# Kernel tuning notes

Hardware: AMD Instinct MI355X
Metric: run time of the kernel (lower is better)

The kernel has to match this reference:

```python
import jax, jax.numpy as jnp
import numpy as np

OUTLINER_RATIO = 0.01
RANK = 16
SVD_NITER = 2  # matches torch.svd_lowrank default


def _randomized_svd(A, rank, key, niter=SVD_NITER):
    # torch.svd_lowrank-style randomized range finder + small SVD.
    n, d = A.shape
    Omega = jax.random.normal(key, (d, rank), dtype=A.dtype)
    Q, _ = jnp.linalg.qr(A @ Omega)               # [n, rank]
    for _ in range(niter):
        Q, _ = jnp.linalg.qr(A.T @ Q)             # [d, rank]
        Q, _ = jnp.linalg.qr(A @ Q)               # [n, rank]
    B = Q.T @ A                                   # [rank, d]
    Ub, S, Vh = jnp.linalg.svd(B, full_matrices=False)
    U = Q @ Ub                                    # [n, rank]
    return U, S, Vh


def get_statistics(x, outliner_ratio):
    # threshold such that ~outliner_ratio fraction of |x| exceeds it
    return jnp.quantile(jnp.abs(x), 1.0 - outliner_ratio)


def compress(x, outliner, rank, key):
    # split outliers (kept exactly) from sub-outlier part (low-rank compressed)
    x_outlier = jnp.where(jnp.abs(x) > outliner, x, jnp.zeros((), x.dtype))
    x_sub = (x - x_outlier).reshape(-1, x.shape[-1])   # [N, D]
    U, S, Vh = _randomized_svd(x_sub, rank, key)
    R = Vh.T                                           # [D, rank]
    Rinv = Vh                                          # orthonormal -> pinv = transpose
    L = x_sub @ R                                      # [N, rank]
    return x_outlier, L, R, Rinv


def reference(x, iteration):
    result = jax.nn.silu(x)
    # iteration < 10 branch: compute fresh outlier statistics
    outliner = get_statistics(x, OUTLINER_RATIO)
    # iteration % 50 == 0 -> execute_svd = True (iteration = 0 here)
    key = jax.random.key(42)
    x_outlier_compressed, L, R, Rinv = compress(x, outliner, RANK, key)
    return result, outliner, R, Rinv


def setup_inputs() -> dict:
    key = jax.random.key(0)
    x = jax.random.normal(key, (4, 2048, 4096), dtype=jnp.float32)
    return {"x": x, "iteration": 0}
```

## Files before the change

kernel.cpp:

```cpp
#include <hip/hip_runtime.h>
#include <math.h>


#define N_TOTAL 33554432
#define DDIM    4096
#define NROWS   8192
#define NCHUNK  32
#define RTARGET 33218888u

__device__ __forceinline__ double frcp(double x){
  double r = (double)(1.0f/(float)x);
  r = r*(2.0 - x*r);
  r = r*(2.0 - x*r);
  return r;
}
__device__ __forceinline__ double frsqrt(double x){
  double r = (double)rsqrtf((float)x);
  double hx = 0.5*x;
  r = r*(1.5 - hx*r*r);
  r = r*(1.5 - hx*r*r);
  return r;
}
__device__ __forceinline__ double fsqrt(double x){
  return (x == 0.0) ? 0.0 : x*frsqrt(x);
}

__device__ __forceinline__ double dsign(double a, double b){ return (b >= 0.0) ? fabs(a) : -fabs(a); }

__device__ __forceinline__ void f_slartg(double f, double g, double& c, double& s, double& r){
  if (g == 0.0){ c=1.0; s=0.0; r=f; }
  else if (f == 0.0){ c=0.0; s=dsign(1.0,g); r=fabs(g); }
  else {
    double d2 = f*f+g*g;
    double inv = frsqrt(d2);
    c = fabs(f)*inv;
    r = dsign(d2*inv, f);
    s = g*inv*dsign(1.0,f);
  }
}

__device__ void f_slas2(double f, double g, double h, double& ssmin, double& ssmax){
  double fa=fabs(f), ga=fabs(g), ha=fabs(h);
  double fhmn=fmin(fa,ha), fhmx=fmax(fa,ha);
  if (fhmn == 0.0){
    ssmin=0.0;
    if (fhmx==0.0) ssmax=ga;
    else { double mx=fmax(fhmx,ga), mn=fmin(fhmx,ga); double q=mn*frcp(mx); ssmax = mx*fsqrt(1.0+q*q); }
  } else {
    if (ga < fhmx){
      double rinv = frcp(fhmx);
      double as_=1.0+fhmn*rinv, at=(fhmx-fhmn)*rinv, au=ga*rinv; au=au*au;
      double c=2.0*frcp(fsqrt(as_*as_+au)+fsqrt(at*at+au));
      ssmin=fhmn*c; ssmax=fhmx*frcp(c);
    } else {
      double au=fhmx*frcp(ga);
      if (au==0.0){ ssmin=(fhmn*fhmx)*frcp(ga); ssmax=ga; }
      else {
        double rinv = frcp(fhmx);
        double as_=1.0+fhmn*rinv, at=(fhmx-fhmn)*rinv;
        double c=frcp(fsqrt(1.0+(as_*au)*(as_*au))+fsqrt(1.0+(at*au)*(at*au)));
        ssmin=(fhmn*c)*au; ssmin=ssmin+ssmin; ssmax=ga*frcp(c+c);
      }
    }
  }
}

__device__ void f_slasv2(double f, double g, double h,
                         double& ssmin, double& ssmax, double& snr, double& csr, double& snl, double& csl){
  const double EPSd = 5.9604645e-8;
  double ft=f, fa=fabs(f), ht=h, ha=fabs(h);
  int pmax=1;
  bool swap_=(ha>fa);
  if (swap_){ pmax=3; double t=ft; ft=ht; ht=t; t=fa; fa=ha; ha=t; }
  double gt=g, ga=fabs(g);
  double clt=0, crt=0, slt=0, srt=0;
  if (ga == 0.0){ ssmin=ha; ssmax=fa; clt=1; crt=1; slt=0; srt=0; }
  else {
    bool gasmal=true;
    if (ga > fa){
      pmax=2;
      if ((fa*frcp(ga)) < EPSd){
        gasmal=false;
        ssmax=ga;
        ssmin = (ha>1.0) ? (fa*frcp(ga*frcp(ha))) : ((fa*frcp(ga))*ha);
        clt=1; slt=ht*frcp(gt); srt=1; crt=ft*frcp(gt);
      }
    }
    if (gasmal){
      double d_=fa-ha;
      double fainv = frcp(fa);
      double l_=(d_==fa)?1.0:(d_*fainv);
      double m_=gt*frcp(ft);
      double t_=2.0-l_;
      double mm=m_*m_, tt=t_*t_;
      double s_=fsqrt(tt+mm);
      double r_=(l_==0.0)?fabs(m_):fsqrt(l_*l_+mm);
      double a_=0.5*(s_+r_);
      double ainv = frcp(a_);
      ssmin=ha*ainv;
      ssmax=fa*a_;
      if (mm==0.0){
        t_=(l_==0.0)?(dsign(2.0,ft)*dsign(1.0,gt)):(gt*frcp(dsign(d_,ft))+m_*frcp(t_));
      } else {
        t_=(m_*frcp(s_+t_)+m_*frcp(r_+l_))*(1.0+a_);
      }
      l_=fsqrt(t_*t_+4.0);
      double linv = frcp(l_);
      crt=2.0*linv;
      srt=t_*linv;
      clt=(crt+srt*m_)*ainv;
      slt=(ht*frcp(ft))*srt*ainv;
    }
  }
  if (swap_){ csl=srt; snl=crt; csr=slt; snr=clt; }
  else { csl=clt; snl=slt; csr=crt; snr=srt; }
  double tsign=0.0;
  if (pmax==1) tsign = dsign(1.0,csr)*dsign(1.0,csl)*dsign(1.0,f);
  if (pmax==2) tsign = dsign(1.0,snr)*dsign(1.0,csl)*dsign(1.0,g);
  if (pmax==3) tsign = dsign(1.0,snr)*dsign(1.0,snl)*dsign(1.0,h);
  ssmax = dsign(ssmax, tsign);
  ssmin = dsign(ssmin, tsign*dsign(1.0,f)*dsign(1.0,h));
}

__global__ __launch_bounds__(256) void k_hist1(const float4* __restrict__ x4, unsigned* __restrict__ h1){
  __shared__ unsigned lh[4096];
  for (int i=threadIdx.x; i<4096; i+=256) lh[i]=0u;
  __syncthreads();
  int tid = blockIdx.x*blockDim.x + threadIdx.x;
  int stride = gridDim.x*blockDim.x;
  for (int i = tid; i < N_TOTAL/4; i += stride){
    float4 v = x4[i];
    atomicAdd(&lh[(__float_as_uint(v.x)&0x7FFFFFFFu)>>19], 1u);
    atomicAdd(&lh[(__float_as_uint(v.y)&0x7FFFFFFFu)>>19], 1u);
    atomicAdd(&lh[(__float_as_uint(v.z)&0x7FFFFFFFu)>>19], 1u);
    atomicAdd(&lh[(__float_as_uint(v.w)&0x7FFFFFFFu)>>19], 1u);
  }
  __syncthreads();
  for (int i=threadIdx.x; i<4096; i+=256){ unsigned c=lh[i]; if (c) atomicAdd(&h1[i], c); }
}

__global__ __launch_bounds__(1024) void k_select1(const unsigned* __restrict__ h1, unsigned* __restrict__ sel){
  __shared__ unsigned ssum[1024];
  int t = threadIdx.x;
  unsigned psum = 0;
  for (int k=0;k<4;++k) psum += h1[t*4+k];
  ssum[t]=psum; __syncthreads();
  for (int off=1; off<1024; off<<=1){
    unsigned v = (t>=off)? ssum[t-off]:0u;
    __syncthreads();
    ssum[t] += v;
    __syncthreads();
  }
  unsigned incl = ssum[t], excl = incl - psum;
  if (excl <= RTARGET && RTARGET < incl){
    unsigned run = excl;
    for (int k=0;k<4;++k){
      unsigned c = h1[t*4+k];
      if (run + c > RTARGET){ sel[1]=(unsigned)(t*4+k); sel[2]=RTARGET-run; break; }
      run += c;
    }
  }
}

__global__ void k_hist2(const float4* __restrict__ x4, unsigned* __restrict__ h2, const unsigned* __restrict__ sel){
  unsigned hstar = sel[1];
  int tid = blockIdx.x*blockDim.x + threadIdx.x;
  int stride = gridDim.x*blockDim.x;
  for (int i = tid; i < N_TOTAL/4; i += stride){
    float4 v = x4[i];
    unsigned b;
    b = __float_as_uint(v.x) & 0x7FFFFFFFu; if ((b>>19)==hstar) atomicAdd(&h2[b&0x7FFFFu],1u);
    b = __float_as_uint(v.y) & 0x7FFFFFFFu; if ((b>>19)==hstar) atomicAdd(&h2[b&0x7FFFFu],1u);
    b = __float_as_uint(v.z) & 0x7FFFFFFFu; if ((b>>19)==hstar) atomicAdd(&h2[b&0x7FFFFu],1u);
    b = __float_as_uint(v.w) & 0x7FFFFFFFu; if ((b>>19)==hstar) atomicAdd(&h2[b&0x7FFFFu],1u);
  }
}

__global__ __launch_bounds__(128) void k_grpsum(const uint4* __restrict__ h2v, unsigned* __restrict__ gs){
  __shared__ unsigned red[128];
  int g = blockIdx.x, t = threadIdx.x;
  uint4 v = h2v[(size_t)g*128 + t];
  red[t] = v.x+v.y+v.z+v.w;
  __syncthreads();
  for (int off=64; off; off>>=1){ if (t<off) red[t] += red[t+off]; __syncthreads(); }
  if (t==0) gs[g] = red[0];
}

__global__ __launch_bounds__(1024) void k_select2b(const unsigned* __restrict__ gs, const unsigned* __restrict__ h2,
                                                   unsigned* __restrict__ sel, float* __restrict__ outScalar){
  __shared__ unsigned ssum[1024];
  __shared__ unsigned sg[2];
  int t = threadIdx.x;
  unsigned target = sel[2], hstar = sel[1];
  unsigned psum = gs[t];
  ssum[t]=psum; __syncthreads();
  for (int off=1; off<1024; off<<=1){
    unsigned v = (t>=off)? ssum[t-off]:0u;
    __syncthreads();
    ssum[t] += v;
    __syncthreads();
  }
  unsigned incl = ssum[t], excl = incl - psum;
  if (excl <= target && target < incl){ sg[0]=(unsigned)t; sg[1]=excl; }
  __syncthreads();
  unsigned g = sg[0], gexcl = sg[1];
  unsigned cnt = (t<512) ? h2[(size_t)g*512 + t] : 0u;
  __syncthreads();
  ssum[t]=cnt; __syncthreads();
  for (int off=1; off<1024; off<<=1){
    unsigned v = (t>=off)? ssum[t-off]:0u;
    __syncthreads();
    ssum[t] += v;
    __syncthreads();
  }
  unsigned incl2 = ssum[t], excl2 = incl2 - cnt;
  unsigned rem = target - gexcl;
  if (t < 512 && excl2 <= rem && rem < incl2){
    unsigned tb = (hstar<<19) | (g*512 + (unsigned)t);
    float tv = __uint_as_float(tb);
    ((float*)sel)[0] = tv;
    *outScalar = tv;
  }
}

__device__ __forceinline__ unsigned rotl32(unsigned x, int r){ return (x<<r)|(x>>(32-r)); }

__device__ __forceinline__ float bits_to_normal(unsigned g){
  float u01 = __uint_as_float((g>>9) | 0x3F800000u) - 1.0f;
  float u = __fadd_rn(__fmul_rn(u01, 2.0f), -0.99999994f);
  u = fmaxf(-0.99999994f, u);
  float xx = __fmul_rn(u,u);
  float w = -log1pf(-xx);
  float p;
  if (w < 5.0f){
    w = __fadd_rn(w, -2.5f);
    p = 2.81022636e-08f;
    p = __fadd_rn(3.43273939e-07f, __fmul_rn(p,w));
    p = __fadd_rn(-3.5233877e-06f, __fmul_rn(p,w));
    p = __fadd_rn(-4.39150654e-06f, __fmul_rn(p,w));
    p = __fadd_rn(0.00021858087f, __fmul_rn(p,w));
    p = __fadd_rn(-0.00125372503f, __fmul_rn(p,w));
    p = __fadd_rn(-0.00417768164f, __fmul_rn(p,w));
    p = __fadd_rn(0.246640727f, __fmul_rn(p,w));
    p = __fadd_rn(1.50140941f, __fmul_rn(p,w));
  } else {
    w = __fadd_rn(sqrtf(w), -3.0f);
    p = -0.000200214257f;
    p = __fadd_rn(0.000100950558f, __fmul_rn(p,w));
    p = __fadd_rn(0.00134934322f, __fmul_rn(p,w));
    p = __fadd_rn(-0.00367342844f, __fmul_rn(p,w));
    p = __fadd_rn(0.00573950773f, __fmul_rn(p,w));
    p = __fadd_rn(-0.0076224613f, __fmul_rn(p,w));
    p = __fadd_rn(0.00943887047f, __fmul_rn(p,w));
    p = __fadd_rn(1.00167406f, __fmul_rn(p,w));
    p = __fadd_rn(2.83297682f, __fmul_rn(p,w));
  }
  return __fmul_rn(__uint_as_float(0x3FB504F3u), __fmul_rn(p,u));
}

#define TF_ROUND(r) { x0 += x1; x1 = rotl32(x1,(r)); x1 ^= x0; }

__global__ void k_omega(float* __restrict__ om){
  unsigned p = blockIdx.x*blockDim.x + threadIdx.x;
  unsigned x0 = p, x1 = 32768u + p;
  const unsigned ks0 = 0u, ks1 = 42u, ks2 = 0x1BD11BDAu ^ 0u ^ 42u;
  x0 += ks0; x1 += ks1;
  TF_ROUND(13) TF_ROUND(15) TF_ROUND(26) TF_ROUND(6)   x0+=ks1; x1+=ks2+1u;
  TF_ROUND(17) TF_ROUND(29) TF_ROUND(16) TF_ROUND(24)  x0+=ks2; x1+=ks0+2u;
  TF_ROUND(13) TF_ROUND(15) TF_ROUND(26) TF_ROUND(6)   x0+=ks0; x1+=ks1+3u;
  TF_ROUND(17) TF_ROUND(29) TF_ROUND(16) TF_ROUND(24)  x0+=ks1; x1+=ks2+4u;
  TF_ROUND(13) TF_ROUND(15) TF_ROUND(26) TF_ROUND(6)   x0+=ks2; x1+=ks0+5u;
  om[p]         = bits_to_normal(x0);
  om[p+32768u]  = bits_to_normal(x1);
}

__global__ __launch_bounds__(256) void k_gemmA(const float* __restrict__ x, const float* __restrict__ W,
                                               float* __restrict__ Y, const float* __restrict__ sel){
  __shared__ double xs[16][128];
  __shared__ double ws[128][16];
  const float t = sel[0];
  const int tid = threadIdx.x;
  const int c = tid & 15, rl = tid >> 4;
  const int row0 = blockIdx.x*16;
  const int c8 = c*8;
  const int wk = (tid*8) >> 4, wc = (tid*8) & 15;
  double acc = 0.0;
  for (int kt = 0; kt < DDIM; kt += 128){
    const float4* p = (const float4*)(x + (size_t)(row0+rl)*DDIM + kt + c8);
    float4 a = p[0], b = p[1];
    xs[rl][c8+0] = (fabsf(a.x) > t) ? 0.0 : (double)a.x;
    xs[rl][c8+1] = (fabsf(a.y) > t) ? 0.0 : (double)a.y;
    xs[rl][c8+2] = (fabsf(a.z) > t) ? 0.0 : (double)a.z;
    xs[rl][c8+3] = (fabsf(a.w) > t) ? 0.0 : (double)a.w;
    xs[rl][c8+4] = (fabsf(b.x) > t) ? 0.0 : (double)b.x;
    xs[rl][c8+5] = (fabsf(b.y) > t) ? 0.0 : (double)b.y;
    xs[rl][c8+6] = (fabsf(b.z) > t) ? 0.0 : (double)b.z;
    xs[rl][c8+7] = (fabsf(b.w) > t) ? 0.0 : (double)b.w;
    const float4* q = (const float4*)(W + (size_t)kt*16 + tid*8);
    float4 wa = q[0], wb = q[1];
    ws[wk][wc+0]=(double)wa.x; ws[wk][wc+1]=(double)wa.y; ws[wk][wc+2]=(double)wa.z; ws[wk][wc+3]=(double)wa.w;
    ws[wk][wc+4]=(double)wb.x; ws[wk][wc+5]=(double)wb.y; ws[wk][wc+6]=(double)wb.z; ws[wk][wc+7]=(double)wb.w;
    __syncthreads();
    #pragma unroll 8
    for (int k=0;k<128;++k) acc += xs[rl][k]*ws[k][c];
    __syncthreads();
  }
  Y[(size_t)(row0+rl)*16 + c] = (float)acc;
}

__global__ __launch_bounds__(256) void k_gemmAT(const float* __restrict__ x, const float* __restrict__ Q,
                                                double* __restrict__ part, const float* __restrict__ sel){
  __shared__ double qs[128][16];
  const float t = sel[0];
  const int tid = threadIdx.x;
  const int d = blockIdx.x*256 + tid;
  const int chunk = blockIdx.y;
  const int i0 = chunk*(NROWS/NCHUNK);
  double acc[16];
  #pragma unroll
  for (int c=0;c<16;++c) acc[c]=0.0;
  for (int it=0; it<NROWS/NCHUNK; it+=128){
    {
      const float4* src = (const float4*)(Q + (size_t)(i0+it)*16) + tid*2;
      float4 a = src[0], b = src[1];
      double* dst = &qs[0][0] + tid*8;
      dst[0]=(double)a.x; dst[1]=(double)a.y; dst[2]=(double)a.z; dst[3]=(double)a.w;
      dst[4]=(double)b.x; dst[5]=(double)b.y; dst[6]=(double)b.z; dst[7]=(double)b.w;
    }
    __syncthreads();
    for (int ii=0; ii<128; ++ii){
      float xv = x[(size_t)(i0+it+ii)*DDIM + d];
      xv = (fabsf(xv) > t) ? 0.0f : xv;
      double xd = (double)xv;
      #pragma unroll
      for (int c=0;c<16;++c) acc[c] += xd*qs[ii][c];
    }
    __syncthreads();
  }
  double* pp = part + ((size_t)chunk*DDIM + d)*16;
  #pragma unroll
  for (int c=0;c<16;++c) pp[c]=acc[c];
}

__global__ void k_reduceT(const double* __restrict__ part, float* __restrict__ outM, int asB, int nchunks){
  int idx = blockIdx.x*blockDim.x + threadIdx.x;
  if (idx >= DDIM*16) return;
  double s = 0.0;
  for (int c=0;c<nchunks;++c) s += part[(size_t)c*DDIM*16 + idx];
  int d = idx >> 4, r = idx & 15;
  if (asB) outM[(size_t)r*DDIM + d] = (float)s;
  else     outM[idx] = (float)s;
}

__global__ __launch_bounds__(256) void k_gramM(const float* __restrict__ M, int rowsPerChunk,
                                               double* __restrict__ part){
  __shared__ float lds[16][17];
  int t = threadIdx.x; int i = t>>4, j = t&15;
  int r0 = blockIdx.x*rowsPerChunk;
  double acc = 0.0;
  for (int rt=0; rt<rowsPerChunk; rt+=16){
    lds[t>>4][t&15] = M[(size_t)(r0+rt+(t>>4))*16 + (t&15)];
    __syncthreads();
    #pragma unroll
    for (int dd=0; dd<16; ++dd) acc += (double)lds[dd][i]*(double)lds[dd][j];
    __syncthreads();
  }
  part[(size_t)blockIdx.x*256 + t] = acc;
}

__global__ __launch_bounds__(256) void k_gramB(const float* __restrict__ B, double* __restrict__ part){
  __shared__ float lds[16][17];
  int t = threadIdx.x; int i = t>>4, j = t&15;
  int d0 = blockIdx.x*256;
  double acc = 0.0;
  for (int dt=0; dt<256; dt+=16){
    lds[t>>4][t&15] = B[(size_t)(t>>4)*DDIM + d0+dt+(t&15)];
    __syncthreads();
    #pragma unroll
    for (int dd=0; dd<16; ++dd) acc += (double)lds[i][dd]*(double)lds[j][dd];
    __syncthreads();
  }
  part[(size_t)blockIdx.x*256 + t] = acc;
}

__global__ __launch_bounds__(256) void k_redchol(const double* __restrict__ part, int nchunks,
                                                 double* __restrict__ Lout, double* __restrict__ Uinv){
  __shared__ double Gs[16][17];
  __shared__ double Vs[16][17];
  int t = threadIdx.x;
  {
    double s = 0.0;
    for (int c=0;c<nchunks;++c) s += part[(size_t)c*256 + t];
    Gs[t>>4][t&15] = s;
  }
  __syncthreads();
  int l = t;
  for (int k=0;k<16;++k){
    if (l==k) Gs[k][k] = fsqrt(Gs[k][k]);
    __syncthreads();
    if (l>k && l<16) Gs[k][l] = Gs[k][l]*frcp(Gs[k][k]);
    __syncthreads();
    if (l>k && l<16){
      double g = Gs[k][l];
      for (int i=k+1;i<=l;++i) Gs[i][l] -= Gs[k][i]*g;
    }
    __syncthreads();
  }
  if (l<16){
    for (int i=0;i<16;++i) Vs[i][l] = 0.0;
    Vs[l][l] = frcp(Gs[l][l]);
    for (int i=l-1;i>=0;--i){
      double s = 0.0;
      for (int k=i+1;k<=l;++k) s += Gs[i][k]*Vs[k][l];
      Vs[i][l] = -s*frcp(Gs[i][i]);
    }
  }
  __syncthreads();
  if (l<16){
    for (int c=0;c<16;++c){
      Lout[l*16+c] = (c<=l) ? Gs[c][l] : 0.0;
      Uinv[l*16+c] = (l<=c) ? Vs[l][c] : 0.0;
    }
  }
}

__global__ __launch_bounds__(256) void k_applyRinv(float* __restrict__ M, const double* __restrict__ Uinv){
  __shared__ double su[256];
  int t = threadIdx.x;
  su[t] = Uinv[t];
  int r = blockIdx.x*16 + (t>>4);
  int j = t & 15;
  const float4* rp = (const float4*)(M + (size_t)r*16);
  float4 v0=rp[0], v1=rp[1], v2=rp[2], v3=rp[3];
  float rowv[16] = {v0.x,v0.y,v0.z,v0.w, v1.x,v1.y,v1.z,v1.w,
                    v2.x,v2.y,v2.z,v2.w, v3.x,v3.y,v3.z,v3.w};
  __syncthreads();
  double acc = 0.0;
  #pragma unroll
  for (int k=0;k<16;++k) acc += (double)rowv[k]*su[k*16+j];
  M[(size_t)r*16 + j] = (float)acc;
}

__global__ __launch_bounds__(64) void k_smallsvd(const double* __restrict__ Lg, double* __restrict__ Wout){
  __shared__ double Lm[16][16];
  __shared__ double VT[16][16];
  __shared__ double A1[16][16];
  __shared__ double dd[16], ee[16], tp[16];
  int l = threadIdx.x;
  for (int idx=l; idx<256; idx+=64){ int r=idx>>4, c=idx&15; Lm[r][c] = (c<=r)? Lg[r*16+c] : 0.0; }
  __syncthreads();
  for (int i=0;i<16;++i){
    double xn2=0.0;
    for (int r=i+1;r<16;++r){ double v=Lm[r][i]; xn2 += v*v; }
    double alpha = Lm[i][i];
    double beta, tauq_, scl;
    if (xn2==0.0){ tauq_=0.0; beta=alpha; scl=0.0; }
    else { beta = -dsign(fsqrt(alpha*alpha+xn2), alpha); tauq_=(beta-alpha)*frcp(beta); scl=frcp(alpha-beta); }
    __syncthreads();
    if (l>i && l<16) Lm[l][i] *= scl;
    __syncthreads();
    dd[i]=beta;
    if (tauq_ != 0.0 && l>i && l<16){
      int j=l;
      double w = Lm[i][j];
      for (int r=i+1;r<16;++r) w += Lm[r][i]*Lm[r][j];
      w *= tauq_;
      Lm[i][j] -= w;
      for (int r=i+1;r<16;++r) Lm[r][j] -= w*Lm[r][i];
    }
    __syncthreads();
    if (i<15){
      double xn2b=0.0;
      for (int c=i+2;c<16;++c){ double v=Lm[i][c]; xn2b+=v*v; }
      double alpha2=Lm[i][i+1];
      double beta2, taup_, scl2;
      if (xn2b==0.0){ taup_=0.0; beta2=alpha2; scl2=0.0; }
      else { beta2=-dsign(fsqrt(alpha2*alpha2+xn2b),alpha2); taup_=(beta2-alpha2)*frcp(beta2); scl2=frcp(alpha2-beta2); }
      __syncthreads();
      if (l>=i+2 && l<16) Lm[i][l] *= scl2;
      __syncthreads();
      ee[i]=beta2; tp[i]=taup_;
      if (taup_!=0.0 && l>i && l<16){
        int r=l;
        double w=Lm[r][i+1];
        for (int c=i+2;c<16;++c) w += Lm[i][c]*Lm[r][c];
        w *= taup_;
        Lm[r][i+1] -= w;
        for (int c=i+2;c<16;++c) Lm[r][c] -= w*Lm[i][c];
      }
      __syncthreads();
    } else { tp[i]=0.0; __syncthreads(); }
  }
  for (int idx=l; idx<256; idx+=64){ int r=idx>>4,c=idx&15; VT[r][c]=(r==c)?1.0:0.0; }
  __syncthreads();
  const double EPSs = 5.9604645e-8;
  const double UNFL = 1.17549435e-38;
  double tol = 10.0*EPSs;
  double sminoa, mu;
  sminoa = mu = fabs(dd[0]);
  if (sminoa != 0.0){
    for (int k=1;k<16;++k){ mu = fabs(dd[k])*(mu*frcp(mu+fabs(ee[k-1]))); sminoa=fmin(sminoa,mu); if (sminoa==0.0) break; }
  }
  sminoa = sminoa/4.0;
  double thresh = fmax(tol*sminoa, 6.0*16.0*16.0*UNFL);
  int m=16, oldll=-1, oldm=-1, idir=0;
  double sminl=0.0;
  int guard=0;
  #define Dv(k) dd[(k)-1]
  #define Ev(k) ee[(k)-1]
  while (m > 1 && guard < 3000){
    ++guard;
    int ll=0; bool split=false;
    double smax_=fabs(Dv(m)), smin_=smax_;
    for (int lll=1; lll<=m-1; ++lll){
      ll = m-lll;
      double abss=fabs(Dv(ll)), abse=fabs(Ev(ll));
      if (abse <= thresh){ split=true; break; }
      smin_=fmin(smin_,abss); smax_=fmax(smax_,fmax(abss,abse));
    }
    if (!split) ll=0;
    else {
      Ev(ll)=0.0;
      if (ll == m-1){ m = m-1; continue; }
    }
    ll = ll+1;
    if (ll == m-1){
      double sigmn,sigmx,sinr,cosr,sinl_,cosl;
      f_slasv2(Dv(m-1), Ev(m-1), Dv(m), sigmn, sigmx, sinr, cosr, sinl_, cosl);
      Dv(m-1)=sigmx; Ev(m-1)=0.0; Dv(m)=sigmn;
      if (l<16){
        double t0 = cosr*VT[m-2][l] + sinr*VT[m-1][l];
        VT[m-1][l] = cosr*VT[m-1][l] - sinr*VT[m-2][l];
        VT[m-2][l] = t0;
      }
      __syncthreads();
      m -= 2; continue;
    }
    if (ll > oldm || m < oldll) idir = (fabs(Dv(ll)) >= fabs(Dv(m))) ? 1 : 2;
    bool cont=false;
    if (idir==1){
      if (fabs(Ev(m-1)) <= tol*fabs(Dv(m))){ Ev(m-1)=0.0; continue; }
      mu = fabs(Dv(ll)); sminl=mu;
      for (int lll=ll; lll<=m-1; ++lll){
        if (fabs(Ev(lll)) <= tol*mu){ Ev(lll)=0.0; cont=true; break; }
        mu = fabs(Dv(lll+1))*(mu*frcp(mu+fabs(Ev(lll)))); sminl=fmin(sminl,mu);
      }
    } else {
      if (fabs(Ev(ll)) <= tol*fabs(Dv(ll))){ Ev(ll)=0.0; continue; }
      mu = fabs(Dv(m)); sminl=mu;
      for (int lll=m-1; lll>=ll; --lll){
        if (fabs(Ev(lll)) <= tol*mu){ Ev(lll)=0.0; cont=true; break; }
        mu = fabs(Dv(lll))*(mu*frcp(mu+fabs(Ev(lll)))); sminl=fmin(sminl,mu);
      }
    }
    if (cont) continue;
    oldll=ll; oldm=m;
    double shift=0.0, rdum;
    if (!( 16.0*tol*(sminl*frcp(smax_)) <= fmax(EPSs, 0.01*tol) )){
      double sll;
      if (idir==1){ sll=fabs(Dv(ll)); f_slas2(Dv(m-1), Ev(m-1), Dv(m), shift, rdum); }
      else        { sll=fabs(Dv(m));  f_slas2(Dv(ll), Ev(ll), Dv(ll+1), shift, rdum); }
      if (sll>0.0){ double q=shift*frcp(sll); if (q*q < EPSs) shift=0.0; }
    }
    if (shift == 0.0){
      if (idir==1){
        double cs=1.0, oldcs=1.0, oldsn=0.0, r_;
        for (int i1=ll;i1<=m-1;++i1){
          double cn, snn;
          double a0 = Dv(i1)*cs;
          f_slartg(a0, Ev(i1), cn, snn, r_);
          if (i1>ll) Ev(i1-1) = oldsn*r_;
          double ocn, osn, dnew;
          f_slartg(oldcs*r_, Dv(i1+1)*snn, ocn, osn, dnew);
          Dv(i1)=dnew;
          cs=cn; oldcs=ocn; oldsn=osn;
          if (l<16){
            double t0 = cs*VT[i1-1][l] + snn*VT[i1][l];
            VT[i1][l] = cs*VT[i1][l] - snn*VT[i1-1][l];
            VT[i1-1][l] = t0;
          }
        }
        double h=Dv(m)*cs;
        Dv(m)=h*oldcs; Ev(m-1)=h*oldsn;
        if (fabs(Ev(m-1))<=thresh) Ev(m-1)=0.0;
      } else {
        double cs=1.0, oldcs=1.0, oldsn=0.0, r_;
        for (int i1=m;i1>=ll+1;--i1){
          double cn,snn;
          double a0 = Dv(i1)*cs;
          f_slartg(a0, Ev(i1-1), cn, snn, r_);
          if (i1<m) Ev(i1)=oldsn*r_;
          double ocn,osn,dnew;
          f_slartg(oldcs*r_, Dv(i1-1)*snn, ocn, osn, dnew);
          Dv(i1)=dnew;
          cs=cn; oldcs=ocn; oldsn=osn;
          if (l<16){
            double c_=oldcs, s_=-oldsn;
            double t0 = c_*VT[i1-2][l] + s_*VT[i1-1][l];
            VT[i1-1][l] = c_*VT[i1-1][l] - s_*VT[i1-2][l];
            VT[i1-2][l] = t0;
          }
        }
        double h=Dv(ll)*cs;
        Dv(ll)=h*oldcs; Ev(ll)=h*oldsn;
        if (fabs(Ev(ll))<=thresh) Ev(ll)=0.0;
      }
    } else {
      if (idir==1){
        double f=(fabs(Dv(ll))-shift)*(dsign(1.0,Dv(ll))+shift*frcp(Dv(ll)));
        double g=Ev(ll);
        for (int i1=ll;i1<=m-1;++i1){
          double cosr,sinr,cosl,sinl_,r_;
          f_slartg(f,g,cosr,sinr,r_);
          if (i1>ll) Ev(i1-1)=r_;
          f = cosr*Dv(i1)+sinr*Ev(i1);
          Ev(i1) = cosr*Ev(i1)-sinr*Dv(i1);
          g = sinr*Dv(i1+1);
          Dv(i1+1) = cosr*Dv(i1+1);
          f_slartg(f,g,cosl,sinl_,r_);
          Dv(i1)=r_;
          f = cosl*Ev(i1)+sinl_*Dv(i1+1);
          Dv(i1+1) = cosl*Dv(i1+1)-sinl_*Ev(i1);
          if (i1 < m-1){ g = sinl_*Ev(i1+1); Ev(i1+1)=cosl*Ev(i1+1); }
          if (l<16){
            double t0 = cosr*VT[i1-1][l] + sinr*VT[i1][l];
            VT[i1][l] = cosr*VT[i1][l] - sinr*VT[i1-1][l];
            VT[i1-1][l] = t0;
          }
        }
        Ev(m-1)=f;
        if (fabs(Ev(m-1))<=thresh) Ev(m-1)=0.0;
      } else {
        double f=(fabs(Dv(m))-shift)*(dsign(1.0,Dv(m))+shift*frcp(Dv(m)));
        double g=Ev(m-1);
        for (int i1=m;i1>=ll+1;--i1){
          double cosr,sinr,cosl,sinl_,r_;
          f_slartg(f,g,cosr,sinr,r_);
          if (i1<m) Ev(i1)=r_;
          f = cosr*Dv(i1)+sinr*Ev(i1-1);
          Ev(i1-1)=cosr*Ev(i1-1)-sinr*Dv(i1);
          g = sinr*Dv(i1-1);
          Dv(i1-1)=cosr*Dv(i1-1);
          f_slartg(f,g,cosl,sinl_,r_);
          Dv(i1)=r_;
          f = cosl*Ev(i1-1)+sinl_*Dv(i1-1);
          Dv(i1-1)=cosl*Dv(i1-1)-sinl_*Ev(i1-1);
          if (i1 > ll+1){ g=sinl_*Ev(i1-2); Ev(i1-2)=cosl*Ev(i1-2); }
          if (l<16){
            double c_=cosr, s_=-sinr;
            double t0 = c_*VT[i1-2][l] + s_*VT[i1-1][l];
            VT[i1-1][l] = c_*VT[i1-1][l] - s_*VT[i1-2][l];
            VT[i1-2][l] = t0;
          }
        }
        Ev(ll)=f;
        if (fabs(Ev(ll))<=thresh) Ev(ll)=0.0;
      }
    }
    __syncthreads();
  }
  __syncthreads();
  for (int k=1;k<=16;++k){
    if (Dv(k) < 0.0){
      Dv(k) = -Dv(k);
      if (l<16) VT[k-1][l] = -VT[k-1][l];
    }
    __syncthreads();
  }
  for (int i1=1;i1<=15;++i1){
    int isub=1; double smn=Dv(1);
    for (int j=2;j<=17-i1;++j){ if (Dv(j) <= smn){ isub=j; smn=Dv(j);} }
    if (isub != 17-i1){
      double tmpd = Dv(17-i1);
      __syncthreads();
      Dv(isub)=tmpd; Dv(17-i1)=smn;
      if (l<16){ double t2=VT[isub-1][l]; VT[isub-1][l]=VT[16-i1][l]; VT[16-i1][l]=t2; }
    }
    __syncthreads();
  }
  for (int i=14;i>=0;--i){
    double tpv = tp[i];
    if (tpv != 0.0 && l<16){
      int r=l;
      double w = VT[r][i+1];
      for (int c=i+2;c<16;++c) w += VT[r][c]*Lm[i][c];
      w *= tpv;
      VT[r][i+1] -= w;
      for (int c=i+2;c<16;++c) VT[r][c] -= w*Lm[i][c];
    }
    __syncthreads();
  }
  if (l<16){
    int r=l;
    for (int j=15;j>=0;--j){
      double s = VT[r][j];
      for (int k=j+1;k<16;++k) s -= A1[r][k]*Lg[k*16+j];
      A1[r][j] = s*frcp(Lg[j*16+j]);
    }
    for (int j=0;j<16;++j) Wout[r*16+j] = A1[r][j];
  }
  #undef Dv
  #undef Ev
}

__global__ __launch_bounds__(256) void k_formVh2(const float* __restrict__ B, const double* __restrict__ W,
                                                 float* __restrict__ outR, float* __restrict__ outRinv){
  __shared__ double sW[256];
  int t = threadIdx.x;
  sW[t] = W[t];
  __syncthreads();
  int d = blockIdx.x*256 + t;
  double bi[16];
  #pragma unroll
  for (int i=0;i<16;++i) bi[i] = (double)B[(size_t)i*DDIM + d];
  #pragma unroll
  for (int r=0;r<16;++r){
    double s = 0.0;
    #pragma unroll
    for (int i=0;i<16;++i) s += sW[r*16+i]*bi[i];
    float f = (float)s;
    outRinv[(size_t)r*DDIM + d] = f;
    outR[(size_t)d*16 + r] = f;
  }
}

__global__ void k_silu(const float4* __restrict__ x4, float4* __restrict__ o4){
  int tid = blockIdx.x*blockDim.x + threadIdx.x;
  int stride = gridDim.x*blockDim.x;
  for (int i = tid; i < N_TOTAL/4; i += stride){
    float4 v = x4[i];
    float4 o;
    o.x = v.x / (1.0f + expf(-v.x));
    o.y = v.y / (1.0f + expf(-v.y));
    o.z = v.z / (1.0f + expf(-v.z));
    o.w = v.w / (1.0f + expf(-v.w));
    o4[i] = o;
  }
}

static void cholQR(float* M, int N, double* partG, double* Ld, double* Uinvd, hipStream_t stream){
  k_gramM<<<32,256,0,stream>>>(M, N/32, partG);
  k_redchol<<<1,256,0,stream>>>(partG, 32, Ld, Uinvd);
  k_applyRinv<<<N/16,256,0,stream>>>(M, Uinvd);
}

extern "C" void kernel_launch(void* const* d_in, const int* in_sizes, int n_in,
                              void* d_out, int out_size, void* d_ws, size_t ws_size,
                              hipStream_t stream) {
  (void)in_sizes; (void)n_in; (void)d_ws; (void)ws_size; (void)out_size;
  const float* x = (const float*)d_in[0];
  float* out = (float*)d_out;
  unsigned* h1   = (unsigned*)out;
  unsigned* h2   = (unsigned*)(out + 4096);
  unsigned* selu = (unsigned*)(out + 528384);
  float*    self = (float*)selu;
  unsigned* gs   = (unsigned*)(out + 528480);
  float* Om = out + 532480;
  float* Y  = out + 598016;
  float* T  = out + 729088;
  float* B  = out + 794624;
  double* dsm  = (double*)(out + 860176);
  double* Ld   = dsm;
  double* Uinvd= dsm + 256;
  double* Wd   = dsm + 512;
  double* part = (double*)(out + 917504);
  double* partG= (double*)(out + 5111808);
  float* outScalar = out + (size_t)N_TOTAL;
  float* outR      = out + (size_t)N_TOTAL + 1;
  float* outRinv   = out + (size_t)N_TOTAL + 1 + 65536;

  hipMemsetAsync(h1, 0, (4096+524288)*sizeof(unsigned), stream);
  k_hist1<<<1024,256,0,stream>>>((const float4*)x, h1);
  k_select1<<<1,1024,0,stream>>>(h1, selu);
  k_hist2<<<2048,256,0,stream>>>((const float4*)x, h2, selu);
  k_grpsum<<<1024,128,0,stream>>>((const uint4*)h2, gs);
  k_select2b<<<1,1024,0,stream>>>(gs, h2, selu, outScalar);
  k_omega<<<128,256,0,stream>>>(Om);

  k_gemmA<<<512,256,0,stream>>>(x, Om, Y, self);
  cholQR(Y, NROWS, partG, Ld, Uinvd, stream);
  for (int it=0; it<2; ++it){
    k_gemmAT<<<dim3(16,NCHUNK),256,0,stream>>>(x, Y, part, self);
    k_reduceT<<<256,256,0,stream>>>(part, T, 0, NCHUNK);
    cholQR(T, DDIM, partG, Ld, Uinvd, stream);
    k_gemmA<<<512,256,0,stream>>>(x, T, Y, self);
    cholQR(Y, NROWS, partG, Ld, Uinvd, stream);
  }
  k_gemmAT<<<dim3(16,NCHUNK),256,0,stream>>>(x, Y, part, self);
  k_reduceT<<<256,256,0,stream>>>(part, B, 1, NCHUNK);
  k_gramB<<<16,256,0,stream>>>(B, partG);
  k_redchol<<<1,256,0,stream>>>(partG, 16, Ld, Uinvd);
  k_smallsvd<<<1,64,0,stream>>>(Ld, Wd);
  k_formVh2<<<16,256,0,stream>>>(B, Wd, outR, outRinv);
  k_silu<<<2048,256,0,stream>>>((const float4*)x, (float4*)out);
}
```

Measured before the change: 1.273 ms.

## Fuse SiLU into first histogram pass and defer Givens updates in small SVD

After: 1.261 ms. About the same (-0.9%).

```diff
diff --git a/kernel.cpp b/kernel.cpp
--- a/kernel.cpp
+++ b/kernel.cpp
@@ -130,6 +130,30 @@
   int stride = gridDim.x*blockDim.x;
   for (int i = tid; i < N_TOTAL/4; i += stride){
     float4 v = x4[i];
+    atomicAdd(&lh[(__float_as_uint(v.x)&0x7FFFFFFFu)>>19], 1u);
+    atomicAdd(&lh[(__float_as_uint(v.y)&0x7FFFFFFFu)>>19], 1u);
+    atomicAdd(&lh[(__float_as_uint(v.z)&0x7FFFFFFFu)>>19], 1u);
+    atomicAdd(&lh[(__float_as_uint(v.w)&0x7FFFFFFFu)>>19], 1u);
+  }
+  __syncthreads();
+  for (int i=threadIdx.x; i<4096; i+=256){ unsigned c=lh[i]; if (c) atomicAdd(&h1[i], c); }
+}
+
+__global__ __launch_bounds__(256) void k_siluhist(const float4* __restrict__ x4, float4* __restrict__ o4,
+                                                  unsigned* __restrict__ h1){
+  __shared__ unsigned lh[4096];
+  for (int i=threadIdx.x; i<4096; i+=256) lh[i]=0u;
+  __syncthreads();
+  int tid = blockIdx.x*blockDim.x + threadIdx.x;
+  int stride = gridDim.x*blockDim.x;
+  for (int i = tid; i < N_TOTAL/4; i += stride){
+    float4 v = x4[i];
+    float4 o;
+    o.x = v.x / (1.0f + expf(-v.x));
+    o.y = v.y / (1.0f + expf(-v.y));
+    o.z = v.z / (1.0f + expf(-v.z));
+    o.w = v.w / (1.0f + expf(-v.w));
+    o4[i] = o;
     atomicAdd(&lh[(__float_as_uint(v.x)&0x7FFFFFFFu)>>19], 1u);
     atomicAdd(&lh[(__float_as_uint(v.y)&0x7FFFFFFFu)>>19], 1u);
     atomicAdd(&lh[(__float_as_uint(v.z)&0x7FFFFFFFu)>>19], 1u);
@@ -446,6 +470,7 @@
   __shared__ double VT[16][16];
   __shared__ double A1[16][16];
   __shared__ double dd[16], ee[16], tp[16];
+  __shared__ double csv[16], snv[16];
   int l = threadIdx.x;
   for (int idx=l; idx<256; idx+=64){ int r=idx>>4, c=idx&15; Lm[r][c] = (c<=r)? Lg[r*16+c] : 0.0; }
   __syncthreads();
@@ -565,96 +590,140 @@
     if (shift == 0.0){
       if (idir==1){
         double cs=1.0, oldcs=1.0, oldsn=0.0, r_;
+        double dcur = Dv(ll);
         for (int i1=ll;i1<=m-1;++i1){
           double cn, snn;
-          double a0 = Dv(i1)*cs;
+          double a0 = dcur*cs;
           f_slartg(a0, Ev(i1), cn, snn, r_);
           if (i1>ll) Ev(i1-1) = oldsn*r_;
+          double dnx = Dv(i1+1);
           double ocn, osn, dnew;
-          f_slartg(oldcs*r_, Dv(i1+1)*snn, ocn, osn, dnew);
+          f_slartg(oldcs*r_, dnx*snn, ocn, osn, dnew);
           Dv(i1)=dnew;
           cs=cn; oldcs=ocn; oldsn=osn;
-          if (l<16){
-            double t0 = cs*VT[i1-1][l] + snn*VT[i1][l];
-            VT[i1][l] = cs*VT[i1][l] - snn*VT[i1-1][l];
-            VT[i1-1][l] = t0;
-          }
+          csv[i1-1]=cs; snv[i1-1]=snn;
+          dcur = dnx;
         }
-        double h=Dv(m)*cs;
+        double h=dcur*cs;
         Dv(m)=h*oldcs; Ev(m-1)=h*oldsn;
         if (fabs(Ev(m-1))<=thresh) Ev(m-1)=0.0;
+        __syncthreads();
+        if (l<16){
+          double v = VT[ll-1][l];
+          for (int i1=ll;i1<=m-1;++i1){
+            double c=csv[i1-1], s=snv[i1-1];
+            double w = VT[i1][l];
+            VT[i1-1][l] = c*v + s*w;
+            v = c*w - s*v;
+          }
+          VT[m-1][l] = v;
+        }
       } else {
         double cs=1.0, oldcs=1.0, oldsn=0.0, r_;
+        double dcur = Dv(m);
         for (int i1=m;i1>=ll+1;--i1){
           double cn,snn;
-          double a0 = Dv(i1)*cs;
+          double a0 = dcur*cs;
           f_slartg(a0, Ev(i1-1), cn, snn, r_);
           if (i1<m) Ev(i1)=oldsn*r_;
+          double dnx = Dv(i1-1);
           double ocn,osn,dnew;
-          f_slartg(oldcs*r_, Dv(i1-1)*snn, ocn, osn, dnew);
+          f_slartg(oldcs*r_, dnx*snn, ocn, osn, dnew);
           Dv(i1)=dnew;
           cs=cn; oldcs=ocn; oldsn=osn;
-          if (l<16){
-            double c_=oldcs, s_=-oldsn;
-            double t0 = c_*VT[i1-2][l] + s_*VT[i1-1][l];
-            VT[i1-1][l] = c_*VT[i1-1][l] - s_*VT[i1-2][l];
-            VT[i1-2][l] = t0;
-          }
+          csv[i1-2]=oldcs; snv[i1-2]=-oldsn;
+          dcur = dnx;
         }
-        double h=Dv(ll)*cs;
+        double h=dcur*cs;
         Dv(ll)=h*oldcs; Ev(ll)=h*oldsn;
         if (fabs(Ev(ll))<=thresh) Ev(ll)=0.0;
+        __syncthreads();
+        if (l<16){
+          double v = VT[m-1][l];
+          for (int i1=m;i1>=ll+1;--i1){
+            double c=csv[i1-2], s=snv[i1-2];
+            double w = VT[i1-2][l];
+            VT[i1-1][l] = c*v - s*w;
+            v = c*w + s*v;
+          }
+          VT[ll-1][l] = v;
+        }
       }
     } else {
       if (idir==1){
         double f=(fabs(Dv(ll))-shift)*(dsign(1.0,Dv(ll))+shift*frcp(Dv(ll)));
         double g=Ev(ll);
+        double dcur = Dv(ll), ecur = Ev(ll);
+        double r_;
         for (int i1=ll;i1<=m-1;++i1){
-          double cosr,sinr,cosl,sinl_,r_;
+          double cosr,sinr,cosl,sinl_;
+          double dnx = Dv(i1+1);
           f_slartg(f,g,cosr,sinr,r_);
           if (i1>ll) Ev(i1-1)=r_;
-          f = cosr*Dv(i1)+sinr*Ev(i1);
-          Ev(i1) = cosr*Ev(i1)-sinr*Dv(i1);
-          g = sinr*Dv(i1+1);
-          Dv(i1+1) = cosr*Dv(i1+1);
+          f = cosr*dcur + sinr*ecur;
+          double e_mid = cosr*ecur - sinr*dcur;
+          g = sinr*dnx;
+          double d_mid = cosr*dnx;
           f_slartg(f,g,cosl,sinl_,r_);
           Dv(i1)=r_;
-          f = cosl*Ev(i1)+sinl_*Dv(i1+1);
-          Dv(i1+1) = cosl*Dv(i1+1)-sinl_*Ev(i1);
-          if (i1 < m-1){ g = sinl_*Ev(i1+1); Ev(i1+1)=cosl*Ev(i1+1); }
-          if (l<16){
-            double t0 = cosr*VT[i1-1][l] + sinr*VT[i1][l];
-            VT[i1][l] = cosr*VT[i1][l] - sinr*VT[i1-1][l];
-            VT[i1-1][l] = t0;
-          }
+          f = cosl*e_mid + sinl_*d_mid;
+          double d_fin = cosl*d_mid - sinl_*e_mid;
+          double e_fin = 0.0;
+          if (i1 < m-1){ double enx = Ev(i1+1); g = sinl_*enx; e_fin = cosl*enx; }
+          csv[i1-1]=cosr; snv[i1-1]=sinr;
+          dcur = d_fin; ecur = e_fin;
         }
+        Dv(m) = dcur;
         Ev(m-1)=f;
         if (fabs(Ev(m-1))<=thresh) Ev(m-1)=0.0;
+        __syncthreads();
+        if (l<16){
+          double v = VT[ll-1][l];
+          for (int i1=ll;i1<=m-1;++i1){
+            double c=csv[i1-1], s=snv[i1-1];
+            double w = VT[i1][l];
+            VT[i1-1][l] = c*v + s*w;
+            v = c*w - s*v;
+          }
+          VT[m-1][l] = v;
+        }
       } else {
         double f=(fabs(Dv(m))-shift)*(dsign(1.0,Dv(m))+shift*frcp(Dv(m)));
         double g=Ev(m-1);
+        double dcur = Dv(m), ecur = Ev(m-1);
+        double r_;
         for (int i1=m;i1>=ll+1;--i1){
-          double cosr,sinr,cosl,sinl_,r_;
+          double cosr,sinr,cosl,sinl_;
+          double dnx = Dv(i1-1);
           f_slartg(f,g,cosr,sinr,r_);
           if (i1<m) Ev(i1)=r_;
-          f = cosr*Dv(i1)+sinr*Ev(i1-1);
-          Ev(i1-1)=cosr*Ev(i1-1)-sinr*Dv(i1);
-          g = sinr*Dv(i1-1);
-          Dv(i1-1)=cosr*Dv(i1-1);
+          f = cosr*dcur + sinr*ecur;
+          double e_mid = cosr*ecur - sinr*dcur;
+          g = sinr*dnx;
+          double d_mid = cosr*dnx;
           f_slartg(f,g,cosl,sinl_,r_);
           Dv(i1)=r_;
-          f = cosl*Ev(i1-1)+sinl_*Dv(i1-1);
-          Dv(i1-1)=cosl*Dv(i1-1)-sinl_*Ev(i1-1);
-          if (i1 > ll+1){ g=sinl_*Ev(i1-2); Ev(i1-2)=cosl*Ev(i1-2); }
-          if (l<16){
-            double c_=cosr, s_=-sinr;
-            double t0 = c_*VT[i1-2][l] + s_*VT[i1-1][l];
-            VT[i1-1][l] = c_*VT[i1-1][l] - s_*VT[i1-2][l];
-            VT[i1-2][l] = t0;
-          }
+          f = cosl*e_mid + sinl_*d_mid;
+          double d_fin = cosl*d_mid - sinl_*e_mid;
+          double e_fin = 0.0;
+          if (i1 > ll+1){ double enx = Ev(i1-2); g = sinl_*enx; e_fin = cosl*enx; }
+          csv[i1-2]=cosr; snv[i1-2]=-sinr;
+          dcur = d_fin; ecur = e_fin;
         }
+        Dv(ll) = dcur;
         Ev(ll)=f;
         if (fabs(Ev(ll))<=thresh) Ev(ll)=0.0;
+        __syncthreads();
+        if (l<16){
+          double v = VT[m-1][l];
+          for (int i1=m;i1>=ll+1;--i1){
+            double c=csv[i1-2], s=snv[i1-2];
+            double w = VT[i1-2][l];
+            VT[i1-1][l] = c*v - s*w;
+            v = c*w + s*v;
+          }
+          VT[ll-1][l] = v;
+        }
       }
     }
     __syncthreads();
@@ -747,30 +816,37 @@
 extern "C" void kernel_launch(void* const* d_in, const int* in_sizes, int n_in,
                               void* d_out, int out_size, void* d_ws, size_t ws_size,
                               hipStream_t stream) {
-  (void)in_sizes; (void)n_in; (void)d_ws; (void)ws_size; (void)out_size;
+  (void)in_sizes; (void)n_in; (void)out_size;
   const float* x = (const float*)d_in[0];
   float* out = (float*)d_out;
-  unsigned* h1   = (unsigned*)out;
-  unsigned* h2   = (unsigned*)(out + 4096);
-  unsigned* selu = (unsigned*)(out + 528384);
+  const size_t NEEDED = 20512768;
+  const bool useWs = (d_ws != nullptr) && (ws_size >= NEEDED);
+  float* scr = useWs ? (float*)d_ws : out;
+  unsigned* h1   = (unsigned*)scr;
+  unsigned* h2   = (unsigned*)(scr + 4096);
+  unsigned* selu = (unsigned*)(scr + 528384);
   float*    self = (float*)selu;
-  unsigned* gs   = (unsigned*)(out + 528480);
-  float* Om = out + 532480;
-  float* Y  = out + 598016;
-  float* T  = out + 729088;
-  float* B  = out + 794624;
-  double* dsm  = (double*)(out + 860176);
+  unsigned* gs   = (unsigned*)(scr + 528480);
+  float* Om = scr + 532480;
+  float* Y  = scr + 598016;
+  float* T  = scr + 729088;
+  float* B  = scr + 794624;
+  double* dsm  = (double*)(scr + 860176);
   double* Ld   = dsm;
   double* Uinvd= dsm + 256;
   double* Wd   = dsm + 512;
-  double* part = (double*)(out + 917504);
-  double* partG= (double*)(out + 5111808);
+  double* part = (double*)(scr + 917504);
+  double* partG= (double*)(scr + 5111808);
   float* outScalar = out + (size_t)N_TOTAL;
   float* outR      = out + (size_t)N_TOTAL + 1;
   float* outRinv   = out + (size_t)N_TOTAL + 1 + 65536;
 
   hipMemsetAsync(h1, 0, (4096+524288)*sizeof(unsigned), stream);
-  k_hist1<<<1024,256,0,stream>>>((const float4*)x, h1);
+  if (useWs){
+    k_siluhist<<<2048,256,0,stream>>>((const float4*)x, (float4*)out, h1);
+  } else {
+    k_hist1<<<1024,256,0,stream>>>((const float4*)x, h1);
+  }
   k_select1<<<1,1024,0,stream>>>(h1, selu);
   k_hist2<<<2048,256,0,stream>>>((const float4*)x, h2, selu);
   k_grpsum<<<1024,128,0,stream>>>((const uint4*)h2, gs);
@@ -792,5 +868,7 @@
   k_redchol<<<1,256,0,stream>>>(partG, 16, Ld, Uinvd);
   k_smallsvd<<<1,64,0,stream>>>(Ld, Wd);
   k_formVh2<<<16,256,0,stream>>>(B, Wd, outR, outRinv);
-  k_silu<<<2048,256,0,stream>>>((const float4*)x, (float4*)out);
-}
+  if (!useWs){
+    k_silu<<<2048,256,0,stream>>>((const float4*)x, (float4*)out);
+  }
+}
```
